# Kernel tuning notes

Measured on AMD Instinct MI355X. Metric: run time of the kernel, lower is better.

The kernel has to match this reference:

```python
import jax, jax.numpy as jnp
import numpy as np

B, S, D = 2, 4096, 512
H, DK, DV = 8, 64, 64
LN_EPS = 1e-5
ATTN_EPS = 1e-6


def layer_norm(x, g, b):
    mu = jnp.mean(x, axis=-1, keepdims=True)
    var = jnp.var(x, axis=-1, keepdims=True)
    return (x - mu) * jax.lax.rsqrt(var + LN_EPS) * g + b


def setup_inputs() -> dict:
    key = jax.random.key(0)
    ks = jax.random.split(key, 12)
    s = 1.0 / np.sqrt(D)
    inp = {
        "Q": jax.random.normal(ks[0], (B, S, D), jnp.float32),
        "K": jax.random.normal(ks[1], (B, S, D), jnp.float32),
        "V": jax.random.normal(ks[2], (B, S, D), jnp.float32),
        "W_q": jax.random.normal(ks[3], (D, H * DK), jnp.float32) * s,
        "W_k": jax.random.normal(ks[4], (D, H * DK), jnp.float32) * s,
        "W_v": jax.random.normal(ks[5], (D, H * DV), jnp.float32) * s,
        "W_o": jax.random.normal(ks[6], (H * DV, D), jnp.float32) * s,
        "ln1_g": jnp.ones((D,), jnp.float32),
        "ln1_b": jnp.zeros((D,), jnp.float32),
        "ln2_g": jnp.ones((D,), jnp.float32),
        "ln2_b": jnp.zeros((D,), jnp.float32),
        "w1": jax.random.normal(ks[7], (4 * D, D), jnp.float32) * s,  # torch Linear: (out, in)
        "b1": jnp.zeros((4 * D,), jnp.float32),
        "w2": jax.random.normal(ks[8], (D, 4 * D), jnp.float32) * (1.0 / np.sqrt(4 * D)),
        "b2": jnp.zeros((D,), jnp.float32),
    }
    return inp


def reference(Q, K, V, W_q, W_k, W_v, W_o, ln1_g, ln1_b, ln2_g, ln2_b, w1, b1, w2, b2):
    Qn = layer_norm(Q, ln1_g, ln1_b)
    # project and split heads: [B,S,H,dk] -> [B,H,S,dk]
    q = (Qn @ W_q).reshape(B, S, H, DK).transpose(0, 2, 1, 3)
    k = (K @ W_k).reshape(B, S, H, DK).transpose(0, 2, 1, 3)
    v = (V @ W_v).reshape(B, S, H, DV).transpose(0, 2, 1, 3)
    scores = jnp.einsum("bhqd,bhkd->bhqk", q, k) / (np.sqrt(DK) + ATTN_EPS)
    attn = jax.nn.softmax(scores, axis=-1)  # same as max-subtract softmax
    ctx = jnp.einsum("bhqk,bhkd->bhqd", attn, v)
    ctx = ctx.transpose(0, 2, 1, 3).reshape(B, S, H * DV)
    att_out = ctx @ W_o  # dropout = identity (eval)
    X = Q + att_out
    Xn = layer_norm(X, ln2_g, ln2_b)
    h = jax.nn.gelu(Xn @ w1.T + b1, approximate=False)
    ffn = h @ w2.T + b2
    return X + ffn
```

## Files before the change

kernel.cpp:

```cpp
#include <hip/hip_runtime.h>

typedef unsigned short u16;
typedef __attribute__((ext_vector_type(8))) short short8;
typedef __attribute__((ext_vector_type(4))) float f32x4;
typedef __attribute__((ext_vector_type(16))) float f32x16;
typedef __attribute__((ext_vector_type(4))) unsigned u32x4;

struct __align__(8) us4 { u16 x, y, z, w; };
struct __align__(8) ui2 { unsigned x, y; };

#define CEXP (1.44269504089f / (8.0f + 1e-6f))

__device__ __forceinline__ u16 f2bf(float f) {
  unsigned u = __builtin_bit_cast(unsigned, f);
  unsigned r = (u + 0x7FFFu + ((u >> 16) & 1u)) >> 16;
  return (u16)r;
}

__device__ __forceinline__ unsigned pack_bf2_trunc(float a, float b) {
  return __builtin_amdgcn_perm(__builtin_bit_cast(unsigned, b),
                               __builtin_bit_cast(unsigned, a), 0x07060302u);
}

__device__ __forceinline__ void async_load16(const void* g, void* l) {
  __builtin_amdgcn_global_load_lds((const __attribute__((address_space(1))) void*)g,
                                   (__attribute__((address_space(3))) void*)l, 16, 0, 0);
}

__global__ void prep_weights(const float* __restrict__ Wq, const float* __restrict__ Wk,
                             const float* __restrict__ Wv, const float* __restrict__ Wo,
                             const float* __restrict__ w1, const float* __restrict__ w2,
                             u16* __restrict__ wqkvT, u16* __restrict__ woT,
                             u16* __restrict__ w1b, u16* __restrict__ w2b) {
  const int z = blockIdx.y;
  const int stride = gridDim.x * blockDim.x;
  const int i0 = blockIdx.x * blockDim.x + threadIdx.x;
  if (z < 4) {
    const float* src = z == 0 ? Wq : z == 1 ? Wk : z == 2 ? Wv : Wo;
    u16* dst = z < 3 ? wqkvT + z * 512 * 512 : woT;
    const float scale = (z == 0) ? CEXP : 1.0f;
    for (int i = i0; i < 512 * 512; i += stride) {
      int n = i >> 9, k = i & 511;
      dst[i] = f2bf(src[k * 512 + n] * scale);
    }
  } else {
    const float* src = z == 4 ? w1 : w2;
    u16* dst = z == 4 ? w1b : w2b;
    for (int i = i0; i < 2048 * 512; i += stride) dst[i] = f2bf(src[i]);
  }
}

template <bool KV>
__launch_bounds__(128)
__global__ void ln_cast(const float* __restrict__ X, const float* __restrict__ gw,
                        const float* __restrict__ bw, u16* __restrict__ Y,
                        const float* __restrict__ Kin, const float* __restrict__ Vin,
                        u16* __restrict__ Kb, u16* __restrict__ Vb) {
  const int row = blockIdx.x, t = threadIdx.x;
  const size_t base = (size_t)row * 512;
  float4 x = ((const float4*)(X + base))[t];
  float s = x.x + x.y + x.z + x.w;
  float ss = x.x * x.x + x.y * x.y + x.z * x.z + x.w * x.w;
#pragma unroll
  for (int off = 32; off > 0; off >>= 1) {
    s += __shfl_xor(s, off);
    ss += __shfl_xor(ss, off);
  }
  __shared__ float red[4];
  if ((t & 63) == 0) { red[(t >> 6) * 2] = s; red[(t >> 6) * 2 + 1] = ss; }
  __syncthreads();
  const float tot = red[0] + red[2], tss = red[1] + red[3];
  const float mu = tot * (1.0f / 512.0f);
  const float var = tss * (1.0f / 512.0f) - mu * mu;
  const float rs = rsqrtf(var + 1e-5f);
  float4 g4 = ((const float4*)gw)[t];
  float4 b4 = ((const float4*)bw)[t];
  us4 o;
  o.x = f2bf((x.x - mu) * rs * g4.x + b4.x);
  o.y = f2bf((x.y - mu) * rs * g4.y + b4.y);
  o.z = f2bf((x.z - mu) * rs * g4.z + b4.z);
  o.w = f2bf((x.w - mu) * rs * g4.w + b4.w);
  ((us4*)(Y + base))[t] = o;
  if constexpr (KV) {
    float4 k4 = ((const float4*)(Kin + base))[t];
    float4 v4 = ((const float4*)(Vin + base))[t];
    us4 ko, vo;
    ko.x = f2bf(k4.x); ko.y = f2bf(k4.y); ko.z = f2bf(k4.z); ko.w = f2bf(k4.w);
    vo.x = f2bf(v4.x); vo.y = f2bf(v4.y); vo.z = f2bf(v4.z); vo.w = f2bf(v4.w);
    ((us4*)(Kb + base))[t] = ko;
    ((us4*)(Vb + base))[t] = vo;
  }
}

__launch_bounds__(256, 3)
__global__ void gemm_qkv(const u16* __restrict__ Aq, const u16* __restrict__ Ak,
                         const u16* __restrict__ Av, const u16* __restrict__ Bt,
                         u16* __restrict__ qb, u16* __restrict__ kb, u16* __restrict__ vtb) {
  __shared__ __align__(16) u16 sA[128 * 32];
  __shared__ __align__(16) u16 sB[128 * 32];
  const int tid = threadIdx.x;
  const int wave = tid >> 6, lane = tid & 63;
  const int l15 = lane & 15, quad = lane >> 4;
  const int qsw = (quad ^ ((l15 >> 1) & 3)) * 8;
  const int m0 = blockIdx.x * 128, n0 = blockIdx.y * 128;
  const int sel = n0 >> 9;
  const u16* A = sel == 0 ? Aq : sel == 1 ? Ak : Av;
  const int wm = (wave >> 1) * 64, wn = (wave & 1) * 64;
  const int u0 = wave * 64 + lane, u1 = u0 + 256;
  const int sw0 = ((u0 & 3) ^ ((u0 >> 3) & 3)) * 8;
  const int K = 512;

  const u16* a0 = A + (size_t)(m0 + (u0 >> 2)) * K + sw0;
  const u16* a1 = A + (size_t)(m0 + (u1 >> 2)) * K + sw0;
  const u16* b0 = Bt + (size_t)(n0 + (u0 >> 2)) * K + sw0;
  const u16* b1p = Bt + (size_t)(n0 + (u1 >> 2)) * K + sw0;

  f32x4 acc[4][4] = {};
  for (int k0 = 0; k0 < K; k0 += 32) {
    async_load16(a0 + k0, &sA[wave * 512]);
    async_load16(a1 + k0, &sA[2048 + wave * 512]);
    async_load16(b0 + k0, &sB[wave * 512]);
    async_load16(b1p + k0, &sB[2048 + wave * 512]);
    __syncthreads();
    short8 af[4], bfr[4];
#pragma unroll
    for (int i = 0; i < 4; i++)
      af[i] = *(const short8*)&sA[(wm + i * 16 + l15) * 32 + qsw];
#pragma unroll
    for (int j = 0; j < 4; j++)
      bfr[j] = *(const short8*)&sB[(wn + j * 16 + l15) * 32 + qsw];
#pragma unroll
    for (int i = 0; i < 4; i++)
#pragma unroll
      for (int j = 0; j < 4; j++)
        acc[i][j] = __builtin_amdgcn_mfma_f32_16x16x32_bf16(af[i], bfr[j], acc[i][j], 0, 0, 0);
    __syncthreads();
  }

#pragma unroll
  for (int i = 0; i < 4; i++) {
#pragma unroll
    for (int j = 0; j < 4; j++) {
      const int ocol = ((n0 + wn) & 511) + j * 16 + l15;
      const int row0 = m0 + wm + i * 16 + quad * 4;
      if (sel == 0) {
#pragma unroll
        for (int r = 0; r < 4; r++) qb[(size_t)(row0 + r) * 512 + ocol] = f2bf(acc[i][j][r]);
      } else if (sel == 1) {
        const int d = ocol & 63, hh2 = ocol >> 6;
        const int ks = d >> 4, hik = (d >> 3) & 1, e = d & 7;
#pragma unroll
        for (int r = 0; r < 4; r++) {
          const int row = row0 + r;
          const int bb = row >> 12, keys = row & 4095;
          const size_t addr =
              (((size_t)((bb * 8 + hh2) * 128 + (keys >> 5)) * 4 + ks) * 64 +
               (keys & 31) + 32 * hik) * 8 + e;
          kb[addr] = f2bf(acc[i][j][r]);
        }
      } else {
        const int b = row0 >> 12, s0 = row0 & 4095;
        const int hh = ocol >> 6, cc = ocol & 63;
        us4 pk;
        pk.x = f2bf(acc[i][j][0]); pk.y = f2bf(acc[i][j][1]);
        pk.z = f2bf(acc[i][j][2]); pk.w = f2bf(acc[i][j][3]);
        *(us4*)&vtb[((size_t)((b * 8 + hh) * 64 + cc) << 12) + s0] = pk;
      }
    }
  }
}

template <int EP, int TN, int LB>
__launch_bounds__(256, LB)
__global__ void gemm_bt(const u16* __restrict__ A, const u16* __restrict__ Bt,
                        int M, int N, int K, void* __restrict__ Cp,
                        const float* __restrict__ bias, const float* __restrict__ res) {
  constexpr int MI = (TN == 128) ? 4 : 2;
  __shared__ __align__(16) u16 sA[128 * 32];
  __shared__ __align__(16) u16 sB[TN * 32];
  const int tid = threadIdx.x;
  const int wave = tid >> 6, lane = tid & 63;
  const int l15 = lane & 15, quad = lane >> 4;
  const int qsw = (quad ^ ((l15 >> 1) & 3)) * 8;
  const int m0 = blockIdx.x * 128, n0 = blockIdx.y * TN;
  const int wm = (TN == 128) ? (wave >> 1) * 64 : wave * 32;
  const int wn = (TN == 128) ? (wave & 1) * 64 : 0;
  const int u0 = wave * 64 + lane, u1 = u0 + 256;
  const int sw0 = ((u0 & 3) ^ ((u0 >> 3) & 3)) * 8;

  const u16* a0 = A + (size_t)(m0 + (u0 >> 2)) * K + sw0;
  const u16* a1 = A + (size_t)(m0 + (u1 >> 2)) * K + sw0;
  const u16* b0 = Bt + (size_t)(n0 + (u0 >> 2)) * K + sw0;

  f32x4 acc[MI][4] = {};
  for (int k0 = 0; k0 < K; k0 += 32) {
    async_load16(a0 + k0, &sA[wave * 512]);
    async_load16(a1 + k0, &sA[2048 + wave * 512]);
    async_load16(b0 + k0, &sB[wave * 512]);
    if constexpr (TN == 128) {
      const u16* b1p = Bt + (size_t)(n0 + (u1 >> 2)) * K + sw0;
      async_load16(b1p + k0, &sB[2048 + wave * 512]);
    }
    __syncthreads();
    short8 af[MI], bfr[4];
#pragma unroll
    for (int i = 0; i < MI; i++)
      af[i] = *(const short8*)&sA[(wm + i * 16 + l15) * 32 + qsw];
#pragma unroll
    for (int j = 0; j < 4; j++)
      bfr[j] = *(const short8*)&sB[(wn + j * 16 + l15) * 32 + qsw];
#pragma unroll
    for (int i = 0; i < MI; i++)
#pragma unroll
      for (int j = 0; j < 4; j++)
        acc[i][j] = __builtin_amdgcn_mfma_f32_16x16x32_bf16(af[i], bfr[j], acc[i][j], 0, 0, 0);
    __syncthreads();
  }

#pragma unroll
  for (int i = 0; i < MI; i++) {
#pragma unroll
    for (int j = 0; j < 4; j++) {
      const int col = n0 + wn + j * 16 + l15;
      const int row0 = m0 + wm + i * 16 + quad * 4;
      if (EP == 2) {
        float* C = (float*)Cp;
#pragma unroll
        for (int r = 0; r < 4; r++) {
          size_t idx = (size_t)(row0 + r) * N + col;
          C[idx] = acc[i][j][r] + res[idx];
        }
      } else if (EP == 3) {
        u16* C = (u16*)Cp;
        const float bv = bias[col];
#pragma unroll
        for (int r = 0; r < 4; r++) {
          float xx = acc[i][j][r] + bv;
          float gl = 0.5f * xx * (1.0f + erff(xx * 0.70710678118f));
          C[(size_t)(row0 + r) * N + col] = f2bf(gl);
        }
      } else {
        float* C = (float*)Cp;
        const float bv = bias[col];
#pragma unroll
        for (int r = 0; r < 4; r++) {
          size_t idx = (size_t)(row0 + r) * N + col;
          C[idx] = acc[i][j][r] + bv + res[idx];
        }
      }
    }
  }
}

__launch_bounds__(512, 2)
__global__ void attn_kernel(const u16* __restrict__ qb, const u16* __restrict__ kfrag,
                            const u16* __restrict__ vtb, u16* __restrict__ ctx) {
  __shared__ __align__(16) u16 smem[16896];
  const int tid = threadIdx.x;
  const int wave = tid >> 6, lane = tid & 63;
  const int l31 = lane & 31, hi = lane >> 5;
  const int qg = wave >> 1, kh = wave & 1;
  const int bh = blockIdx.x, b = bh >> 3, h = bh & 7;
  const int q0 = blockIdx.y * 128;
  const size_t rb = (size_t)b * 4096;
  const int qrow = q0 + qg * 32 + l31;

  short8 qf[4];
#pragma unroll
  for (int ks = 0; ks < 4; ks++)
    qf[ks] = *(const short8*)&qb[(rb + qrow) * 512 + h * 64 + ks * 16 + hi * 8];

  int voff[2][2];
#pragma unroll
  for (int vb = 0; vb < 2; vb++) {
    const int vrow = vb * 32 + l31;
    voff[vb][0] = vrow * 64 + (((kh * 4 + hi) ^ (vrow & 7))) * 8;
    voff[vb][1] = vrow * 64 + (((kh * 4 + 2 + hi) ^ (vrow & 7))) * 8;
  }

  const int srow = tid >> 3, ssl = (tid & 7) ^ (srow & 7);
  const u16* vp = vtb + (size_t)(bh * 64 + srow) * 4096 + ssl * 8;
  const int sdst = tid * 8;

  const u16* kp = kfrag + ((size_t)(bh * 128 + kh) * 4) * 512 + lane * 8;

  short8 kc[4];
  f32x16 ov[2] = {};
  float l_part = 0.f;

#pragma unroll
  for (int ks = 0; ks < 4; ks++) kc[ks] = *(const short8*)(kp + ks * 512);
  kp += 4096;
  async_load16(vp, &smem[sdst]);
  vp += 64;
  asm volatile("s_waitcnt vmcnt(0)" ::: "memory");
  __syncthreads();

#define BODY(VB, COND)                                                              \
  {                                                                                 \
    f32x16 st = {};                                                                 \
    __builtin_amdgcn_s_setprio(1);                                                  \
    _Pragma("unroll") for (int ks = 0; ks < 4; ks++)                                \
      st = __builtin_amdgcn_mfma_f32_32x32x16_bf16(kc[ks], qf[ks], st, 0, 0, 0);    \
    __builtin_amdgcn_s_setprio(0);                                                  \
    if (COND) {                                                                     \
      _Pragma("unroll") for (int ks = 0; ks < 4; ks++)                              \
        kc[ks] = *(const short8*)(kp + ks * 512);                                   \
      kp += 4096;                                                                   \
      async_load16(vp, &smem[(1 - (VB)) * 4096 + sdst]);                            \
      vp += 64;                                                                     \
    }                                                                               \
    float p[16];                                                                    \
    _Pragma("unroll") for (int i = 0; i < 16; i++)                                  \
        p[i] = __builtin_amdgcn_exp2f(st[i]);                                       \
    _Pragma("unroll") for (int i = 0; i < 16; i += 4)                               \
        l_part += (p[i] + p[i + 1]) + (p[i + 2] + p[i + 3]);                        \
    unsigned x0 = pack_bf2_trunc(p[0], p[1]), x1 = pack_bf2_trunc(p[2], p[3]);      \
    unsigned x2 = pack_bf2_trunc(p[4], p[5]), x3 = pack_bf2_trunc(p[6], p[7]);      \
    unsigned x4 = pack_bf2_trunc(p[8], p[9]), x5 = pack_bf2_trunc(p[10], p[11]);    \
    unsigned x6 = pack_bf2_trunc(p[12], p[13]), x7 = pack_bf2_trunc(p[14], p[15]);  \
    auto r0 = __builtin_amdgcn_permlane32_swap(x0, x2, false, false);               \
    auto r1 = __builtin_amdgcn_permlane32_swap(x1, x3, false, false);               \
    auto r2 = __builtin_amdgcn_permlane32_swap(x4, x6, false, false);               \
    auto r3 = __builtin_amdgcn_permlane32_swap(x5, x7, false, false);               \
    u32x4 w0 = {r0[0], r1[0], r0[1], r1[1]};                                        \
    u32x4 w1 = {r2[0], r3[0], r2[1], r3[1]};                                        \
    short8 pf0 = __builtin_bit_cast(short8, w0);                                    \
    short8 pf1 = __builtin_bit_cast(short8, w1);                                    \
    __builtin_amdgcn_s_setprio(1);                                                  \
    _Pragma("unroll") for (int vb = 0; vb < 2; vb++) {                              \
      short8 vf0 = *(const short8*)&smem[(VB) * 4096 + voff[vb][0]];                \
      short8 vf1 = *(const short8*)&smem[(VB) * 4096 + voff[vb][1]];                \
      ov[vb] = __builtin_amdgcn_mfma_f32_32x32x16_bf16(vf0, pf0, ov[vb], 0, 0, 0);  \
      ov[vb] = __builtin_amdgcn_mfma_f32_32x32x16_bf16(vf1, pf1, ov[vb], 0, 0, 0);  \
    }                                                                               \
    __builtin_amdgcn_s_setprio(0);                                                  \
    if (COND) {                                                                     \
      asm volatile("s_waitcnt vmcnt(0)" ::: "memory");                              \
      __syncthreads();                                                              \
    }                                                                               \
  }

  for (int g = 0; g < 32; g++) {
    BODY(0, true);
    BODY(1, (g < 31));
  }
#undef BODY

  float l2 = l_part + __shfl_xor(l_part, 32);
  __syncthreads();
  float* mrg = (float*)smem;
  float* mrgl = (float*)smem + 8192;
  if (kh == 1) {
#pragma unroll
    for (int vb = 0; vb < 2; vb++)
#pragma unroll
      for (int e = 0; e < 16; e++)
        mrg[(qg * 32 + vb * 16 + e) * 64 + lane] = ov[vb][e];
    mrgl[qg * 64 + lane] = l2;
  }
  __syncthreads();
  if (kh == 0) {
    const float inv = 1.0f / (l2 + mrgl[qg * 64 + lane]);
#pragma unroll
    for (int vb = 0; vb < 2; vb++) {
#pragma unroll
      for (int rg = 0; rg < 4; rg++) {
        us4 o;
        o.x = f2bf((ov[vb][rg * 4 + 0] + mrg[(qg * 32 + vb * 16 + rg * 4 + 0) * 64 + lane]) * inv);
        o.y = f2bf((ov[vb][rg * 4 + 1] + mrg[(qg * 32 + vb * 16 + rg * 4 + 1) * 64 + lane]) * inv);
        o.z = f2bf((ov[vb][rg * 4 + 2] + mrg[(qg * 32 + vb * 16 + rg * 4 + 2) * 64 + lane]) * inv);
        o.w = f2bf((ov[vb][rg * 4 + 3] + mrg[(qg * 32 + vb * 16 + rg * 4 + 3) * 64 + lane]) * inv);
        *(us4*)&ctx[(rb + qrow) * 512 + h * 64 + vb * 32 + rg * 8 + hi * 4] = o;
      }
    }
  }
}

extern "C" void kernel_launch(void* const* d_in, const int* in_sizes, int n_in,
                              void* d_out, int out_size, void* d_ws, size_t ws_size,
                              hipStream_t stream) {
  (void)in_sizes; (void)n_in; (void)out_size; (void)ws_size;
  const float* Q = (const float*)d_in[0];
  const float* K = (const float*)d_in[1];
  const float* V = (const float*)d_in[2];
  const float* W_q = (const float*)d_in[3];
  const float* W_k = (const float*)d_in[4];
  const float* W_v = (const float*)d_in[5];
  const float* W_o = (const float*)d_in[6];
  const float* ln1_g = (const float*)d_in[7];
  const float* ln1_b = (const float*)d_in[8];
  const float* ln2_g = (const float*)d_in[9];
  const float* ln2_b = (const float*)d_in[10];
  const float* w1 = (const float*)d_in[11];
  const float* b1 = (const float*)d_in[12];
  const float* w2 = (const float*)d_in[13];
  const float* b2 = (const float*)d_in[14];

  char* w = (char*)d_ws;
  const size_t MB = 1u << 20;
  u16* wqkvT = (u16*)(w);
  u16* woT = (u16*)(w + 3 * MB / 2);
  u16* w1b = (u16*)(w + 2 * MB);
  u16* w2b = (u16*)(w + 4 * MB);
  u16* Qn  = (u16*)(w + 6 * MB);
  u16* Kb  = (u16*)(w + 14 * MB);
  u16* Vb  = (u16*)(w + 22 * MB);
  u16* qb  = (u16*)(w + 30 * MB);
  u16* kb  = (u16*)(w + 38 * MB);
  u16* vtb = (u16*)(w + 46 * MB);
  u16* ctx = (u16*)(w + 54 * MB);
  float* X = (float*)(w + 62 * MB);
  u16* Xn  = (u16*)(w + 6 * MB);
  u16* hb  = (u16*)(w + 14 * MB);

  prep_weights<<<dim3(128, 6), 256, 0, stream>>>(W_q, W_k, W_v, W_o, w1, w2,
                                                 wqkvT, woT, w1b, w2b);
  ln_cast<true><<<8192, 128, 0, stream>>>(Q, ln1_g, ln1_b, Qn, K, V, Kb, Vb);
  gemm_qkv<<<dim3(64, 12), 256, 0, stream>>>(Qn, Kb, Vb, wqkvT, qb, kb, vtb);
  attn_kernel<<<dim3(16, 32), 512, 0, stream>>>(qb, kb, vtb, ctx);
  gemm_bt<2, 64, 3><<<dim3(64, 8), 256, 0, stream>>>(ctx, woT, 8192, 512, 512, X, nullptr, Q);
  ln_cast<false><<<8192, 128, 0, stream>>>(X, ln2_g, ln2_b, Xn, nullptr, nullptr, nullptr, nullptr);
  gemm_bt<3, 128, 3><<<dim3(64, 16), 256, 0, stream>>>(Xn, w1b, 8192, 2048, 512, hb, b1, nullptr);
  gemm_bt<4, 64, 3><<<dim3(64, 8), 256, 0, stream>>>(hb, w2b, 8192, 512, 2048, (float*)d_out, b2, X);
}
```

Baseline: 330.1 us.

## Double K-step per barrier in GEMMs and relax attention vmcnt waits

The GEMM kernels now load two 32-wide K slices into separate LDS buffers per iteration, which halves the number of barrier pairs per K loop and raises LDS use. The attention loop issues the V async load before the K fragment loads and waits with vmcnt(4) instead of vmcnt(0), so the K register loads for the next step can stay in flight across the barrier. It also swaps __syncthreads for a bare s_barrier. The vmcnt(4) count relies on the V load being issued before the four K loads and on the compiler keeping that order; a different order could let the barrier pass before the V tile has landed.

```diff
diff --git a/kernel.cpp b/kernel.cpp
--- a/kernel.cpp
+++ b/kernel.cpp
@@ -96,8 +96,8 @@
 __global__ void gemm_qkv(const u16* __restrict__ Aq, const u16* __restrict__ Ak,
                          const u16* __restrict__ Av, const u16* __restrict__ Bt,
                          u16* __restrict__ qb, u16* __restrict__ kb, u16* __restrict__ vtb) {
-  __shared__ __align__(16) u16 sA[128 * 32];
-  __shared__ __align__(16) u16 sB[128 * 32];
+  __shared__ __align__(16) u16 sA[2][128 * 32];
+  __shared__ __align__(16) u16 sB[2][128 * 32];
   const int tid = threadIdx.x;
   const int wave = tid >> 6, lane = tid & 63;
   const int l15 = lane & 15, quad = lane >> 4;
@@ -116,24 +116,31 @@
   const u16* b1p = Bt + (size_t)(n0 + (u1 >> 2)) * K + sw0;
 
   f32x4 acc[4][4] = {};
-  for (int k0 = 0; k0 < K; k0 += 32) {
-    async_load16(a0 + k0, &sA[wave * 512]);
-    async_load16(a1 + k0, &sA[2048 + wave * 512]);
-    async_load16(b0 + k0, &sB[wave * 512]);
-    async_load16(b1p + k0, &sB[2048 + wave * 512]);
+  for (int k0 = 0; k0 < K; k0 += 64) {
+#pragma unroll
+    for (int hf = 0; hf < 2; hf++) {
+      const int kk = k0 + hf * 32;
+      async_load16(a0 + kk, &sA[hf][wave * 512]);
+      async_load16(a1 + kk, &sA[hf][2048 + wave * 512]);
+      async_load16(b0 + kk, &sB[hf][wave * 512]);
+      async_load16(b1p + kk, &sB[hf][2048 + wave * 512]);
+    }
     __syncthreads();
-    short8 af[4], bfr[4];
-#pragma unroll
-    for (int i = 0; i < 4; i++)
-      af[i] = *(const short8*)&sA[(wm + i * 16 + l15) * 32 + qsw];
-#pragma unroll
-    for (int j = 0; j < 4; j++)
-      bfr[j] = *(const short8*)&sB[(wn + j * 16 + l15) * 32 + qsw];
-#pragma unroll
-    for (int i = 0; i < 4; i++)
+#pragma unroll
+    for (int hf = 0; hf < 2; hf++) {
+      short8 af[4], bfr[4];
+#pragma unroll
+      for (int i = 0; i < 4; i++)
+        af[i] = *(const short8*)&sA[hf][(wm + i * 16 + l15) * 32 + qsw];
 #pragma unroll
       for (int j = 0; j < 4; j++)
-        acc[i][j] = __builtin_amdgcn_mfma_f32_16x16x32_bf16(af[i], bfr[j], acc[i][j], 0, 0, 0);
+        bfr[j] = *(const short8*)&sB[hf][(wn + j * 16 + l15) * 32 + qsw];
+#pragma unroll
+      for (int i = 0; i < 4; i++)
+#pragma unroll
+        for (int j = 0; j < 4; j++)
+          acc[i][j] = __builtin_amdgcn_mfma_f32_16x16x32_bf16(af[i], bfr[j], acc[i][j], 0, 0, 0);
+    }
     __syncthreads();
   }
 
@@ -176,8 +183,8 @@
                         int M, int N, int K, void* __restrict__ Cp,
                         const float* __restrict__ bias, const float* __restrict__ res) {
   constexpr int MI = (TN == 128) ? 4 : 2;
-  __shared__ __align__(16) u16 sA[128 * 32];
-  __shared__ __align__(16) u16 sB[TN * 32];
+  __shared__ __align__(16) u16 sA[2][128 * 32];
+  __shared__ __align__(16) u16 sB[2][TN * 32];
   const int tid = threadIdx.x;
   const int wave = tid >> 6, lane = tid & 63;
   const int l15 = lane & 15, quad = lane >> 4;
@@ -193,27 +200,34 @@
   const u16* b0 = Bt + (size_t)(n0 + (u0 >> 2)) * K + sw0;
 
   f32x4 acc[MI][4] = {};
-  for (int k0 = 0; k0 < K; k0 += 32) {
-    async_load16(a0 + k0, &sA[wave * 512]);
-    async_load16(a1 + k0, &sA[2048 + wave * 512]);
-    async_load16(b0 + k0, &sB[wave * 512]);
-    if constexpr (TN == 128) {
-      const u16* b1p = Bt + (size_t)(n0 + (u1 >> 2)) * K + sw0;
-      async_load16(b1p + k0, &sB[2048 + wave * 512]);
+  for (int k0 = 0; k0 < K; k0 += 64) {
+#pragma unroll
+    for (int hf = 0; hf < 2; hf++) {
+      const int kk = k0 + hf * 32;
+      async_load16(a0 + kk, &sA[hf][wave * 512]);
+      async_load16(a1 + kk, &sA[hf][2048 + wave * 512]);
+      async_load16(b0 + kk, &sB[hf][wave * 512]);
+      if constexpr (TN == 128) {
+        const u16* b1p = Bt + (size_t)(n0 + (u1 >> 2)) * K + sw0;
+        async_load16(b1p + kk, &sB[hf][2048 + wave * 512]);
+      }
     }
     __syncthreads();
-    short8 af[MI], bfr[4];
-#pragma unroll
-    for (int i = 0; i < MI; i++)
-      af[i] = *(const short8*)&sA[(wm + i * 16 + l15) * 32 + qsw];
-#pragma unroll
-    for (int j = 0; j < 4; j++)
-      bfr[j] = *(const short8*)&sB[(wn + j * 16 + l15) * 32 + qsw];
-#pragma unroll
-    for (int i = 0; i < MI; i++)
+#pragma unroll
+    for (int hf = 0; hf < 2; hf++) {
+      short8 af[MI], bfr[4];
+#pragma unroll
+      for (int i = 0; i < MI; i++)
+        af[i] = *(const short8*)&sA[hf][(wm + i * 16 + l15) * 32 + qsw];
 #pragma unroll
       for (int j = 0; j < 4; j++)
-        acc[i][j] = __builtin_amdgcn_mfma_f32_16x16x32_bf16(af[i], bfr[j], acc[i][j], 0, 0, 0);
+        bfr[j] = *(const short8*)&sB[hf][(wn + j * 16 + l15) * 32 + qsw];
+#pragma unroll
+      for (int i = 0; i < MI; i++)
+#pragma unroll
+        for (int j = 0; j < 4; j++)
+          acc[i][j] = __builtin_amdgcn_mfma_f32_16x16x32_bf16(af[i], bfr[j], acc[i][j], 0, 0, 0);
+    }
     __syncthreads();
   }
 
@@ -288,13 +302,14 @@
   f32x16 ov[2] = {};
   float l_part = 0.f;
 
+  async_load16(vp, &smem[sdst]);
+  vp += 64;
+  asm volatile("" ::: "memory");
 #pragma unroll
   for (int ks = 0; ks < 4; ks++) kc[ks] = *(const short8*)(kp + ks * 512);
   kp += 4096;
-  async_load16(vp, &smem[sdst]);
-  vp += 64;
-  asm volatile("s_waitcnt vmcnt(0)" ::: "memory");
-  __syncthreads();
+  asm volatile("s_waitcnt vmcnt(4)" ::: "memory");
+  __builtin_amdgcn_s_barrier();
 
 #define BODY(VB, COND)                                                              \
   {                                                                                 \
@@ -304,11 +319,12 @@
       st = __builtin_amdgcn_mfma_f32_32x32x16_bf16(kc[ks], qf[ks], st, 0, 0, 0);    \
     __builtin_amdgcn_s_setprio(0);                                                  \
     if (COND) {                                                                     \
+      async_load16(vp, &smem[(1 - (VB)) * 4096 + sdst]);                            \
+      vp += 64;                                                                     \
+      asm volatile("" ::: "memory");                                                \
       _Pragma("unroll") for (int ks = 0; ks < 4; ks++)                              \
         kc[ks] = *(const short8*)(kp + ks * 512);                                   \
       kp += 4096;                                                                   \
-      async_load16(vp, &smem[(1 - (VB)) * 4096 + sdst]);                            \
-      vp += 64;                                                                     \
     }                                                                               \
     float p[16];                                                                    \
     _Pragma("unroll") for (int i = 0; i < 16; i++)                                  \
@@ -336,8 +352,8 @@
     }                                                                               \
     __builtin_amdgcn_s_setprio(0);                                                  \
     if (COND) {                                                                     \
-      asm volatile("s_waitcnt vmcnt(0)" ::: "memory");                              \
-      __syncthreads();                                                              \
+      asm volatile("s_waitcnt vmcnt(4)" ::: "memory");                              \
+      __builtin_amdgcn_s_barrier();                                                 \
     }                                                                               \
   }
 
```

After: 311.1 us. -5.8%, faster.
